# Kernel tuning notes

Measured on AMD Instinct MI355X. Metric: run time of the kernel, lower is better.

## Reference

```python
import jax, jax.numpy as jnp
import numpy as np

# Network geometry: 8 layers x 524288 buckets, 8 spigots per bucket (uniform).
L_LAYERS = 8
B_PER_LAYER = 524288
NB = L_LAYERS * B_PER_LAYER      # total buckets = 4_194_304
NS = 8                           # spigots per bucket
G = 9.8                          # gravity constant from module


def setup_inputs() -> dict:
    key = jax.random.key(0)
    k1, k2, k3, k4 = jax.random.split(key, 4)
    # Head starts above all spigot heights (initial_head_in_buckets ~ 2) so h > 0.
    H = 2.0 + jax.random.uniform(k1, (NB,), dtype=jnp.float32)
    # S[..., 0] = spigot height in (0,1); S[..., 1] = spigot area in (0,1).
    S = jax.random.uniform(k2, (NB, NS, 2), dtype=jnp.float32)
    # theta flattened in (layer, bucket, spigot) order -> plain reshape to [NB, NS].
    theta = jax.random.uniform(k3, (NB * NS,), dtype=jnp.float32)
    # precip_into_network_at_update (scalar), unit_precip = 6.0 scale.
    precip = jax.random.uniform(k4, (), dtype=jnp.float32) * 6.0
    return {"H": H, "S": S, "theta": theta, "precip": precip}


def reference(H, S, theta, precip):
    # --- update_spigot_outflow (vectorized over layers/buckets/spigots) ---
    th = theta.reshape(NB, NS)                      # triple loop == reshape
    h = jnp.maximum(0.0, H[:, None] - S[:, :, 0])   # head above spigot
    flow_rate_modifier = 0.5 * (jnp.tanh(h) + 1.0)
    v = th * jnp.sqrt(2.0 * G * h) * flow_rate_modifier
    s_q = v * S[:, :, 1]                            # [NB, NS] spigot outflows

    # --- update_network_fluxes (upstream precip distribution) ---
    outflows = jnp.sum(s_q, axis=1)                 # [NB]
    # inflows[1:] = outflows[:-1]; inflows[0] = precip (upstream)
    inflows = jnp.concatenate([precip[None].astype(H.dtype), outflows[:-1]])

    # --- update_head_in_buckets ---
    H_new = H + inflows - outflows

    # --- set_network_outflow: total outflow of last layer's buckets ---
    network_outflow = jnp.sum(s_q[NB - B_PER_LAYER:])

    return H_new, s_q, network_outflow
```

## Files before the change

### kernel.cpp

```cpp
#include <hip/hip_runtime.h>

#define NL 8
#define BPL 524288
#define NB (NL * BPL)
#define NS 8
#define GRAV 9.8f

__global__ __launch_bounds__(256) void spigot_kernel(
    const float* __restrict__ H,
    const float* __restrict__ S,
    const float* __restrict__ theta,
    float* __restrict__ s_q,
    float* __restrict__ outflows)
{
    const int tid    = blockIdx.x * 256 + threadIdx.x;
    const int bucket = tid >> 3;

    const float  th = theta[tid];
    const float2 sv = reinterpret_cast<const float2*>(S)[tid];
    const float  Hb = H[bucket];

    const float h   = fmaxf(0.0f, Hb - sv.x);
    const float e   = __expf(-2.0f * h);
    const float mod = __builtin_amdgcn_rcpf(1.0f + e);
    const float v   = th * __builtin_amdgcn_sqrtf(2.0f * GRAV * h) * mod;
    const float q   = v * sv.y;

    s_q[tid] = q;

    if (outflows != nullptr) {
        float sum = q;
        sum += __shfl_xor(sum, 1);
        sum += __shfl_xor(sum, 2);
        sum += __shfl_xor(sum, 4);
        if ((threadIdx.x & 7) == 0) outflows[bucket] = sum;
    }
}

__global__ __launch_bounds__(256) void head_kernel(
    const float* __restrict__ H,
    const float* __restrict__ outflows,
    const float* __restrict__ precip,
    float* __restrict__ H_new,
    float* __restrict__ net_out)
{
    const int t = blockIdx.x * 256 + threadIdx.x;
    const int i = t << 2;

    const float4 o  = reinterpret_cast<const float4*>(outflows)[t];
    const float4 Hv = reinterpret_cast<const float4*>(H)[t];
    const float om1 = (i == 0) ? precip[0] : outflows[i - 1];

    float4 hn;
    hn.x = Hv.x + om1 - o.x;
    hn.y = Hv.y + o.x - o.y;
    hn.z = Hv.z + o.y - o.z;
    hn.w = Hv.w + o.z - o.w;
    reinterpret_cast<float4*>(H_new)[t] = hn;

    float part = (o.x + o.y) + (o.z + o.w);
    part += __shfl_xor(part, 1);
    part += __shfl_xor(part, 2);
    part += __shfl_xor(part, 4);
    part += __shfl_xor(part, 8);
    part += __shfl_xor(part, 16);
    part += __shfl_xor(part, 32);

    __shared__ float smem[4];
    const int lane = threadIdx.x & 63;
    const int w    = threadIdx.x >> 6;
    if (lane == 0) smem[w] = part;
    __syncthreads();
    if (threadIdx.x == 0 && blockIdx.x >= ((NB - BPL) >> 10)) {
        atomicAdd(net_out, (smem[0] + smem[1]) + (smem[2] + smem[3]));
    }
}

__global__ __launch_bounds__(256) void head_kernel_nows(
    const float* __restrict__ H,
    const float* __restrict__ s_q,
    const float* __restrict__ precip,
    float* __restrict__ H_new,
    float* __restrict__ net_out)
{
    const int i = blockIdx.x * 256 + threadIdx.x;
    const float4* q4 = reinterpret_cast<const float4*>(s_q);

    const float4 a = q4[i * 2];
    const float4 b = q4[i * 2 + 1];
    const float of = ((a.x + a.y) + (a.z + a.w)) + ((b.x + b.y) + (b.z + b.w));

    float infl;
    if (i == 0) {
        infl = precip[0];
    } else {
        const float4 c = q4[i * 2 - 2];
        const float4 d = q4[i * 2 - 1];
        infl = ((c.x + c.y) + (c.z + c.w)) + ((d.x + d.y) + (d.z + d.w));
    }
    H_new[i] = H[i] + infl - of;

    float part = (i >= NB - BPL) ? of : 0.0f;
    part += __shfl_xor(part, 1);
    part += __shfl_xor(part, 2);
    part += __shfl_xor(part, 4);
    part += __shfl_xor(part, 8);
    part += __shfl_xor(part, 16);
    part += __shfl_xor(part, 32);

    __shared__ float smem[4];
    const int lane = threadIdx.x & 63;
    const int w    = threadIdx.x >> 6;
    if (lane == 0) smem[w] = part;
    __syncthreads();
    if (threadIdx.x == 0 && blockIdx.x >= ((NB - BPL) >> 8)) {
        atomicAdd(net_out, (smem[0] + smem[1]) + (smem[2] + smem[3]));
    }
}

extern "C" void kernel_launch(void* const* d_in, const int* in_sizes, int n_in,
                              void* d_out, int out_size, void* d_ws, size_t ws_size,
                              hipStream_t stream) {
    const float* H      = (const float*)d_in[0];
    const float* S      = (const float*)d_in[1];
    const float* theta  = (const float*)d_in[2];
    const float* precip = (const float*)d_in[3];

    float* out     = (float*)d_out;
    float* H_new   = out;
    float* s_q     = out + NB;
    float* net_out = out + NB + (size_t)NB * NS;

    hipMemsetAsync(net_out, 0, sizeof(float), stream);

    const bool have_ws = (ws_size >= (size_t)NB * sizeof(float));
    float* outflows = have_ws ? (float*)d_ws : nullptr;

    spigot_kernel<<<(NB * NS) / 256, 256, 0, stream>>>(H, S, theta, s_q, outflows);

    if (have_ws) {
        head_kernel<<<NB / 1024, 256, 0, stream>>>(H, outflows, precip, H_new, net_out);
    } else {
        head_kernel_nows<<<NB / 256, 256, 0, stream>>>(H, s_q, precip, H_new, net_out);
    }
}
```

Baseline: 491.3 us.

## Fuse spigot outflow and head update into a single kernel with halo recompute

Merges the spigot kernel and the head-update kernel into one launch. Per-bucket outflows go to shared memory, and each block recomputes the preceding bucket's outflow from its inputs as a halo, so the intermediate outflows array no longer has to round-trip through global memory. The last-layer reduction is also folded in via a block-level atomic. The cost is a small amount of redundant computation and extra loads per block, plus a __syncthreads in the main kernel.

```diff
diff --git a/kernel.cpp b/kernel.cpp
--- a/kernel.cpp
+++ b/kernel.cpp
@@ -6,15 +6,18 @@
 #define NS 8
 #define GRAV 9.8f
 
-__global__ __launch_bounds__(256) void spigot_kernel(
+__global__ __launch_bounds__(256) void fused_kernel(
     const float* __restrict__ H,
     const float* __restrict__ S,
     const float* __restrict__ theta,
+    const float* __restrict__ precip,
     float* __restrict__ s_q,
-    float* __restrict__ outflows)
+    float* __restrict__ H_new,
+    float* __restrict__ net_out)
 {
     const int tid    = blockIdx.x * 256 + threadIdx.x;
     const int bucket = tid >> 3;
+    const int lb     = threadIdx.x >> 3;
 
     const float  th = theta[tid];
     const float2 sv = reinterpret_cast<const float2*>(S)[tid];
@@ -28,93 +31,53 @@
 
     s_q[tid] = q;
 
-    if (outflows != nullptr) {
-        float sum = q;
-        sum += __shfl_xor(sum, 1);
-        sum += __shfl_xor(sum, 2);
-        sum += __shfl_xor(sum, 4);
-        if ((threadIdx.x & 7) == 0) outflows[bucket] = sum;
+    float sum = q;
+    sum += __shfl_xor(sum, 1);
+    sum += __shfl_xor(sum, 2);
+    sum += __shfl_xor(sum, 4);
+
+    __shared__ float bsum[33];
+    __shared__ float wsum[4];
+    if ((threadIdx.x & 7) == 0) bsum[lb + 1] = sum;
+
+    const bool last_layer = (blockIdx.x >= ((NB - BPL) >> 5));
+    if (last_layer) {
+        float part = sum;
+        part += __shfl_xor(part, 8);
+        part += __shfl_xor(part, 16);
+        part += __shfl_xor(part, 32);
+        if ((threadIdx.x & 63) == 0) wsum[threadIdx.x >> 6] = part;
     }
-}
 
-__global__ __launch_bounds__(256) void head_kernel(
-    const float* __restrict__ H,
-    const float* __restrict__ outflows,
-    const float* __restrict__ precip,
-    float* __restrict__ H_new,
-    float* __restrict__ net_out)
-{
-    const int t = blockIdx.x * 256 + threadIdx.x;
-    const int i = t << 2;
+    if (threadIdx.x < 8) {
+        float pq;
+        if (blockIdx.x > 0) {
+            const int   pidx = blockIdx.x * 256 - 8 + threadIdx.x;
+            const float pth  = theta[pidx];
+            const float2 psv = reinterpret_cast<const float2*>(S)[pidx];
+            const float pH   = H[pidx >> 3];
+            const float ph   = fmaxf(0.0f, pH - psv.x);
+            const float pe   = __expf(-2.0f * ph);
+            const float pmod = __builtin_amdgcn_rcpf(1.0f + pe);
+            const float pv   = pth * __builtin_amdgcn_sqrtf(2.0f * GRAV * ph) * pmod;
+            pq = pv * psv.y;
+        } else {
+            pq = (threadIdx.x == 0) ? precip[0] : 0.0f;
+        }
+        pq += __shfl_xor(pq, 1);
+        pq += __shfl_xor(pq, 2);
+        pq += __shfl_xor(pq, 4);
+        if (threadIdx.x == 0) bsum[0] = pq;
+    }
 
-    const float4 o  = reinterpret_cast<const float4*>(outflows)[t];
-    const float4 Hv = reinterpret_cast<const float4*>(H)[t];
-    const float om1 = (i == 0) ? precip[0] : outflows[i - 1];
+    __syncthreads();
 
-    float4 hn;
-    hn.x = Hv.x + om1 - o.x;
-    hn.y = Hv.y + o.x - o.y;
-    hn.z = Hv.z + o.y - o.z;
-    hn.w = Hv.w + o.z - o.w;
-    reinterpret_cast<float4*>(H_new)[t] = hn;
+    if ((threadIdx.x & 7) == 0) {
+        H_new[bucket] = Hb + bsum[lb] - bsum[lb + 1];
+    }
 
-    float part = (o.x + o.y) + (o.z + o.w);
-    part += __shfl_xor(part, 1);
-    part += __shfl_xor(part, 2);
-    part += __shfl_xor(part, 4);
-    part += __shfl_xor(part, 8);
-    part += __shfl_xor(part, 16);
-    part += __shfl_xor(part, 32);
-
-    __shared__ float smem[4];
-    const int lane = threadIdx.x & 63;
-    const int w    = threadIdx.x >> 6;
-    if (lane == 0) smem[w] = part;
-    __syncthreads();
-    if (threadIdx.x == 0 && blockIdx.x >= ((NB - BPL) >> 10)) {
-        atomicAdd(net_out, (smem[0] + smem[1]) + (smem[2] + smem[3]));
-    }
-}
-
-__global__ __launch_bounds__(256) void head_kernel_nows(
-    const float* __restrict__ H,
-    const float* __restrict__ s_q,
-    const float* __restrict__ precip,
-    float* __restrict__ H_new,
-    float* __restrict__ net_out)
-{
-    const int i = blockIdx.x * 256 + threadIdx.x;
-    const float4* q4 = reinterpret_cast<const float4*>(s_q);
-
-    const float4 a = q4[i * 2];
-    const float4 b = q4[i * 2 + 1];
-    const float of = ((a.x + a.y) + (a.z + a.w)) + ((b.x + b.y) + (b.z + b.w));
-
-    float infl;
-    if (i == 0) {
-        infl = precip[0];
-    } else {
-        const float4 c = q4[i * 2 - 2];
-        const float4 d = q4[i * 2 - 1];
-        infl = ((c.x + c.y) + (c.z + c.w)) + ((d.x + d.y) + (d.z + d.w));
-    }
-    H_new[i] = H[i] + infl - of;
-
-    float part = (i >= NB - BPL) ? of : 0.0f;
-    part += __shfl_xor(part, 1);
-    part += __shfl_xor(part, 2);
-    part += __shfl_xor(part, 4);
-    part += __shfl_xor(part, 8);
-    part += __shfl_xor(part, 16);
-    part += __shfl_xor(part, 32);
-
-    __shared__ float smem[4];
-    const int lane = threadIdx.x & 63;
-    const int w    = threadIdx.x >> 6;
-    if (lane == 0) smem[w] = part;
-    __syncthreads();
-    if (threadIdx.x == 0 && blockIdx.x >= ((NB - BPL) >> 8)) {
-        atomicAdd(net_out, (smem[0] + smem[1]) + (smem[2] + smem[3]));
+    if (last_layer && threadIdx.x == 0) {
+        atomicAdd(net_out, (wsum[0] + wsum[1]) + (wsum[2] + wsum[3]));
     }
 }
 
@@ -133,14 +96,6 @@
 
     hipMemsetAsync(net_out, 0, sizeof(float), stream);
 
-    const bool have_ws = (ws_size >= (size_t)NB * sizeof(float));
-    float* outflows = have_ws ? (float*)d_ws : nullptr;
-
-    spigot_kernel<<<(NB * NS) / 256, 256, 0, stream>>>(H, S, theta, s_q, outflows);
-
-    if (have_ws) {
-        head_kernel<<<NB / 1024, 256, 0, stream>>>(H, outflows, precip, H_new, net_out);
-    } else {
-        head_kernel_nows<<<NB / 256, 256, 0, stream>>>(H, s_q, precip, H_new, net_out);
-    }
+    fused_kernel<<<(NB * NS) / 256, 256, 0, stream>>>(
+        H, S, theta, precip, s_q, H_new, net_out);
 }
```

Measured after the change: 699.6 us. 42.4% more time.
